# Kernel tuning notes

Hardware: AMD Instinct MI355X
Metric: run time of the kernel (lower is better)

Reference implementation:

```python
import jax, jax.numpy as jnp
import numpy as np

HEAD, STACK = 8, 2
EPS = 1e-5


def _ln2d(x):
    # F.layer_norm(x, x.size()[1:]): normalize over (seq, feature) jointly, no affine
    m = jnp.mean(x, axis=(1, 2), keepdims=True)
    v = jnp.var(x, axis=(1, 2), keepdims=True)
    return (x - m) / jnp.sqrt(v + EPS)


def setup_inputs() -> dict:
    key = jax.random.key(0)
    ks = jax.random.split(key, 8)
    B, S, V, E, D, C = 64, 1024, 8000, 200, 200, 31
    g = lambda k, shape, sc: (jax.random.normal(k, shape, jnp.float32) * sc)
    return dict(
        x=jax.random.randint(ks[0], (B, S), 0, V),
        embed=g(ks[1], (V, E), 0.02),
        pos=g(ks[2], (S, E), 0.02),
        Wp=g(ks[3], (E, D), 0.05), bp=jnp.zeros((D,), jnp.float32),
        Wm=g(ks[4], (D * HEAD, D), 0.05), bm=jnp.zeros((D,), jnp.float32),
        W1=g(ks[5], (D, D), 0.05), b1=jnp.zeros((D,), jnp.float32),
        W2=g(ks[6], (D, D), 0.05), b2=jnp.zeros((D,), jnp.float32),
        Wd=g(ks[7], (D, C), 0.05), bd=jnp.zeros((C,), jnp.float32),
    )


def reference(x, embed, pos, Wp, bp, Wm, bm, W1, b1, W2, b2, Wd, bd):
    h = embed[x] + pos                       # [B,S,200]
    scale = jnp.sqrt(jnp.asarray(Wp.shape[1], jnp.float32))
    for _ in range(STACK):                   # weights shared across stacks (aliased in torch)
        r = h
        p = h @ Wp + bp                      # q = k = v (same aliased Linear in torch)
        a = jax.nn.softmax(jnp.einsum('bsd,btd->bst', p, p) / scale, axis=-1)
        c = jnp.einsum('bst,btd->bsd', a, p)  # [B,S,200]
        cat = jnp.tile(c, (1, 1, HEAD))       # all heads identical -> concat = tile
        h = _ln2d(cat @ Wm + bm + r)
        r = h
        ff = jax.nn.relu(h @ W1 + b1) @ W2 + b2
        h = _ln2d(ff + r)
    return h[:, -1, :] @ Wd + bd             # [B, class_num]; dropout = identity (eval)
```

## Files before the change

### kernel.cpp

```cpp
#include <hip/hip_runtime.h>
#include <cstddef>
#include <cstdint>
#include <cmath>

#define BDIM  64
#define SDIM  1024
#define DDIM  200
#define DPAD  224
#define PSTRIDE 232
#define CDIM  31
#define NSTACK 2
#define EPS   1e-5f
#define LN_N  204800.0f

typedef __attribute__((ext_vector_type(8))) short short8;
typedef __attribute__((ext_vector_type(4))) short short4_t;
typedef __attribute__((ext_vector_type(4))) float f32x4;

__device__ __forceinline__ short f2bf(float f) {
    union { float f; unsigned u; } v; v.f = f;
    unsigned r = v.u + 0x7FFFu + ((v.u >> 16) & 1u);
    return (short)(r >> 16);
}
__device__ __forceinline__ float bf2f(short s) {
    union { unsigned u; float f; } v; v.u = ((unsigned)(unsigned short)s) << 16;
    return v.f;
}
__device__ __forceinline__ unsigned cvtpk_bf16(float a, float b) {
    unsigned r;
    asm volatile("v_cvt_pk_bf16_f32 %0, %1, %2" : "=v"(r) : "v"(a), "v"(b));
    return r;
}
__device__ __forceinline__ void gload_lds16(const short* g, short* l) {
    __builtin_amdgcn_global_load_lds(
        (const __attribute__((address_space(1))) void*)g,
        (__attribute__((address_space(3))) void*)l, 16, 0, 0);
}

__global__ void prep_kernel(const float* __restrict__ Wp, const float* __restrict__ bp,
                            const float* __restrict__ Wm, const float* __restrict__ bm,
                            const float* __restrict__ W1, const float* __restrict__ b1,
                            const float* __restrict__ W2, const float* __restrict__ b2,
                            short* __restrict__ WtP, short* __restrict__ WtM,
                            short* __restrict__ Wt1, short* __restrict__ Wt2,
                            float* __restrict__ bpP, float* __restrict__ bmP,
                            float* __restrict__ b1P, float* __restrict__ b2P,
                            float* __restrict__ csP, float* __restrict__ cs1)
{
    int idx = blockIdx.x * 256 + threadIdx.x;
    if (idx >= DPAD * DPAD) return;
    int n = idx / DPAD, k = idx - n * DPAD;
    bool valid = (n < DDIM) && (k < DDIM);
    WtP[idx] = valid ? f2bf(Wp[(size_t)k * DDIM + n]) : 0;
    Wt1[idx] = valid ? f2bf(W1[(size_t)k * DDIM + n]) : 0;
    Wt2[idx] = valid ? f2bf(W2[(size_t)k * DDIM + n]) : 0;
    float s = 0.f;
    if (valid) {
        #pragma unroll
        for (int blk = 0; blk < 8; ++blk)
            s += Wm[(size_t)(blk * DDIM + k) * DDIM + n];
    }
    WtM[idx] = valid ? f2bf(s) : 0;
    if (idx < DPAD) {
        bpP[idx] = idx < DDIM ? bp[idx] : 0.f;
        bmP[idx] = idx < DDIM ? bm[idx] : 0.f;
        b1P[idx] = idx < DDIM ? b1[idx] : 0.f;
        b2P[idx] = idx < DDIM ? b2[idx] : 0.f;
        float sp = 0.f, s1 = 0.f;
        if (idx < DDIM) {
            for (int kk = 0; kk < DDIM; ++kk) {
                sp += bf2f(f2bf(Wp[(size_t)kk * DDIM + idx]));
                s1 += bf2f(f2bf(W1[(size_t)kk * DDIM + idx]));
            }
        }
        csP[idx] = sp;
        cs1[idx] = s1;
    }
}

__global__ void embed_kernel(const int* __restrict__ x, const float* __restrict__ embed,
                             const float* __restrict__ pos, short* __restrict__ h)
{
    const int row = blockIdx.x;
    const int n = threadIdx.x;
    if (n >= DPAD) return;
    const int s = row & (SDIM - 1);
    const int tok = x[row];
    float v = (n < DDIM) ? embed[(size_t)tok * DDIM + n] + pos[(size_t)s * DDIM + n] : 0.f;
    h[(size_t)row * DPAD + n] = (n < DDIM) ? f2bf(v) : (short)0;
}

#define WSLICE 7168
#define GBUFSZ 11264
__global__ __launch_bounds__(256, 2)
void gemm_bf(const short* __restrict__ act, const float* __restrict__ actParts,
             const short* __restrict__ Wt, const float* __restrict__ bias,
             const float* __restrict__ csW,
             const short* __restrict__ res, const float* __restrict__ resParts,
             short* __restrict__ out, float* __restrict__ parts,
             int doRelu, int outStride)
{
    __shared__ short SB[2][GBUFSZ];

    const int tid  = threadIdx.x;
    const int wave = tid >> 6, lane = tid & 63;
    const int lo   = lane & 15, hi = lane >> 4;
    const int mblk = blockIdx.x * 128;

    auto stage = [&](int ks, int buf) {
        for (int c = wave; c < 22; c += 4) {
            if (c < 14) {
                int row = c * 16 + (lane >> 2);
                int kc  = (lane & 3) ^ ((row >> 1) & 3);
                gload_lds16(Wt + (size_t)row * DPAD + ks * 32 + kc * 8,
                            &SB[buf][c * 512 + lane * 8]);
            } else {
                int ci  = c - 14;
                int row = ci * 16 + (lane >> 2);
                int kc  = (lane & 3) ^ ((row >> 1) & 3);
                gload_lds16(act + (size_t)(mblk + row) * DPAD + ks * 32 + kc * 8,
                            &SB[buf][WSLICE + ci * 512 + lane * 8]);
            }
        }
    };

    f32x4 acc[2][14];
    #pragma unroll
    for (int mt = 0; mt < 2; ++mt)
        #pragma unroll
        for (int nt = 0; nt < 14; ++nt) acc[mt][nt] = (f32x4){0.f, 0.f, 0.f, 0.f};

    stage(0, 0);
    __syncthreads();

    #pragma unroll
    for (int ks = 0; ks < 7; ++ks) {
        const int cur = ks & 1;
        if (ks < 6) stage(ks + 1, cur ^ 1);

        short8 af[2];
        #pragma unroll
        for (int mt = 0; mt < 2; ++mt) {
            int arow = wave * 32 + mt * 16 + lo;
            af[mt] = *(const short8*)&SB[cur][WSLICE + arow * 32
                                             + ((hi * 8) ^ (((arow >> 1) & 3) << 3))];
        }
        #pragma unroll
        for (int nt = 0; nt < 14; ++nt) {
            int brow = nt * 16 + lo;
            short8 bf_ = *(const short8*)&SB[cur][brow * 32
                                                 + ((hi * 8) ^ (((brow >> 1) & 3) << 3))];
            acc[0][nt] = __builtin_amdgcn_mfma_f32_16x16x32_bf16(af[0], bf_, acc[0][nt], 0, 0, 0);
            acc[1][nt] = __builtin_amdgcn_mfma_f32_16x16x32_bf16(af[1], bf_, acc[1][nt], 0, 0, 0);
        }
        __syncthreads();
    }

    const int bb = mblk >> 10;
    float inv_a = 1.f, corr = 0.f;
    if (actParts) {
        float mean = actParts[bb * 2] / LN_N;
        inv_a = rsqrtf(actParts[bb * 2 + 1] / LN_N - mean * mean + EPS);
        corr = mean * inv_a;
    }
    float mean_r = 0.f, inv_r = 1.f;
    if (resParts) {
        mean_r = resParts[bb * 2] / LN_N;
        inv_r = rsqrtf(resParts[bb * 2 + 1] / LN_N - mean_r * mean_r + EPS);
    }

    float s = 0.f, s2 = 0.f;
    #pragma unroll
    for (int mt = 0; mt < 2; ++mt) {
        #pragma unroll
        for (int nt = 0; nt < 14; ++nt) {
            const int n = nt * 16 + lo;
            const float bn = bias[n];
            const float cw = actParts ? csW[n] : 0.f;
            float v[4];
            #pragma unroll
            for (int r = 0; r < 4; ++r)
                v[r] = acc[mt][nt][r] * inv_a + bn - corr * cw;
            if (res) {
                #pragma unroll
                for (int r = 0; r < 4; ++r) {
                    int m = mblk + wave * 32 + mt * 16 + hi * 4 + r;
                    v[r] += (bf2f(res[(size_t)m * DPAD + n]) - mean_r) * inv_r;
                }
            }
            if (doRelu)
                #pragma unroll
                for (int r = 0; r < 4; ++r) v[r] = fmaxf(v[r], 0.f);
            if (n >= DDIM)
                #pragma unroll
                for (int r = 0; r < 4; ++r) v[r] = 0.f;
            if (parts)
                #pragma unroll
                for (int r = 0; r < 4; ++r) { s += v[r]; s2 = fmaf(v[r], v[r], s2); }
            #pragma unroll
            for (int r = 0; r < 4; ++r) {
                int m = mblk + wave * 32 + mt * 16 + hi * 4 + r;
                out[(size_t)m * outStride + n] = f2bf(v[r]);
            }
        }
    }

    if (parts) {
        __shared__ float rs[4], rq[4];
        #pragma unroll
        for (int off = 32; off; off >>= 1) {
            s  += __shfl_down(s, off);
            s2 += __shfl_down(s2, off);
        }
        if (lane == 0) { rs[wave] = s; rq[wave] = s2; }
        __syncthreads();
        if (tid == 0) {
            atomicAdd(&parts[bb * 2],     rs[0] + rs[1] + rs[2] + rs[3]);
            atomicAdd(&parts[bb * 2 + 1], rq[0] + rq[1] + rq[2] + rq[3]);
        }
    }
}

__global__ void vt_kernel(const short* __restrict__ p, short* __restrict__ pt)
{
    __shared__ short T[32][33];
    const int b  = blockIdx.z;
    const int s0 = blockIdx.x * 32;
    const int d0 = blockIdx.y * 32;
    const int t  = threadIdx.x;
    const int row = t >> 3, c4 = (t & 7) * 4;
    short4_t v = *(const short4_t*)(p + ((size_t)b * SDIM + s0 + row) * PSTRIDE + d0 + c4);
    #pragma unroll
    for (int j = 0; j < 4; ++j) T[row][c4 + j] = v[j];
    __syncthreads();
    short4_t o;
    #pragma unroll
    for (int j = 0; j < 4; ++j) o[j] = T[c4 + j][row];
    *(short4_t*)(pt + ((size_t)b * DPAD + d0 + row) * SDIM + s0 + c4) = o;
}

__global__ __launch_bounds__(256, 2)
void attn_kernel(const short* __restrict__ pbf, const short* __restrict__ pt,
                 short* __restrict__ c, float qscale)
{
    __shared__ short Kbuf[2][7680];
    __shared__ short Vbuf[2][6656];

    const int bid = blockIdx.x;
    const int wg  = (bid & 7) * 64 + (bid >> 3);
    const int b   = wg >> 3;
    const int q0  = (wg & 7) * 128;

    const int tid  = threadIdx.x;
    const int wave = tid >> 6;
    const int lane = tid & 63;
    const int lo   = lane & 15;
    const int hi   = lane >> 4;

    const short* pb  = pbf + (size_t)b * SDIM * PSTRIDE;
    const short* ptb = pt  + (size_t)b * DPAD * SDIM;

    auto stage = [&](int kt2, int bufIdx) {
        const short* ks = pb + (size_t)kt2 * 32 * PSTRIDE + lane * 8;
        #pragma unroll
        for (int i = 0; i < 15; ++i)
            gload_lds16(ks + i * 512, &Kbuf[bufIdx][i * 512]);
        #pragma unroll
        for (int i = 0; i < 13; ++i) {
            int e = i * 512 + lane * 8;
            int d = e >> 5;
            int cc = (e & 31) ^ (((d >> 1) & 3) << 3);
            gload_lds16(ptb + (size_t)d * SDIM + kt2 * 32 + cc, &Vbuf[bufIdx][i * 512]);
        }
    };

    short8 qf[2][7];
    #pragma unroll
    for (int qt = 0; qt < 2; ++qt)
        #pragma unroll
        for (int ks = 0; ks < 7; ++ks) {
            short8 q = *(const short8*)(pb + (size_t)(q0 + wave * 32 + qt * 16 + lo) * PSTRIDE
                                        + ks * 32 + hi * 8);
            short8 qs;
            #pragma unroll
            for (int j = 0; j < 8; ++j) qs[j] = f2bf(bf2f(q[j]) * qscale);
            qf[qt][ks] = qs;
        }

    f32x4 o[2][13];
    float m[2], ell[2];
    #pragma unroll
    for (int qt = 0; qt < 2; ++qt) {
        #pragma unroll
        for (int n = 0; n < 13; ++n) o[qt][n] = (f32x4){0.f, 0.f, 0.f, 0.f};
        m[qt] = -1e30f; ell[qt] = 0.f;
    }

    if (wave == 0) stage(0, 0);
    __syncthreads();

    for (int kt = 0; kt < 32; ++kt) {
        const int cur = kt & 1;
        if (kt < 31 && wave == ((kt + 1) & 3)) stage(kt + 1, cur ^ 1);

        f32x4 sacc[2][2];
        #pragma unroll
        for (int qt = 0; qt < 2; ++qt)
            #pragma unroll
            for (int t = 0; t < 2; ++t) sacc[qt][t] = (f32x4){0.f, 0.f, 0.f, 0.f};
        __builtin_amdgcn_s_setprio(1);
        #pragma unroll
        for (int t = 0; t < 2; ++t)
            #pragma unroll
            for (int ks = 0; ks < 7; ++ks) {
                short8 kf = *(const short8*)(&Kbuf[cur][(t * 16 + lo) * PSTRIDE + ks * 32 + hi * 8]);
                sacc[0][t] = __builtin_amdgcn_mfma_f32_16x16x32_bf16(kf, qf[0][ks], sacc[0][t], 0, 0, 0);
                sacc[1][t] = __builtin_amdgcn_mfma_f32_16x16x32_bf16(kf, qf[1][ks], sacc[1][t], 0, 0, 0);
            }
        __builtin_amdgcn_s_setprio(0);

        short8 pa[2];
        #pragma unroll
        for (int qt = 0; qt < 2; ++qt) {
            float mx = fmaxf(fmaxf(fmaxf(sacc[qt][0][0], sacc[qt][0][1]),
                                   fmaxf(sacc[qt][0][2], sacc[qt][0][3])),
                             fmaxf(fmaxf(sacc[qt][1][0], sacc[qt][1][1]),
                                   fmaxf(sacc[qt][1][2], sacc[qt][1][3])));
            mx = fmaxf(mx, __shfl_xor(mx, 16));
            mx = fmaxf(mx, __shfl_xor(mx, 32));
            if (__any(mx > m[qt] + 11.5f)) {
                float mn = fmaxf(m[qt], mx);
                float al = exp2f(m[qt] - mn);
                m[qt] = mn; ell[qt] *= al;
                float alr[4];
                #pragma unroll
                for (int r = 0; r < 4; ++r) alr[r] = __shfl(al, hi * 4 + r);
                #pragma unroll
                for (int n = 0; n < 13; ++n)
                    #pragma unroll
                    for (int r = 0; r < 4; ++r) o[qt][n][r] *= alr[r];
            }
            float p[2][4]; float rsum = 0.f;
            #pragma unroll
            for (int t = 0; t < 2; ++t)
                #pragma unroll
                for (int r = 0; r < 4; ++r) {
                    p[t][r] = exp2f(sacc[qt][t][r] - m[qt]);
                    rsum += p[t][r];
                }
            rsum += __shfl_xor(rsum, 16);
            rsum += __shfl_xor(rsum, 32);
            ell[qt] += rsum;
            unsigned pk01_0 = cvtpk_bf16(p[0][0], p[0][1]);
            unsigned pk23_0 = cvtpk_bf16(p[0][2], p[0][3]);
            unsigned pk01_1 = cvtpk_bf16(p[1][0], p[1][1]);
            unsigned pk23_1 = cvtpk_bf16(p[1][2], p[1][3]);
            const int srcA = lo + ((hi & 1) * 2) * 16;
            const int srcB = srcA + 16;
            int a0 = __shfl((int)pk01_0, srcA), a1 = __shfl((int)pk01_1, srcA);
            int b0 = __shfl((int)pk23_0, srcA), b1 = __shfl((int)pk23_1, srcA);
            int c0 = __shfl((int)pk01_0, srcB), c1 = __shfl((int)pk01_1, srcB);
            int d0 = __shfl((int)pk23_0, srcB), d1 = __shfl((int)pk23_1, srcB);
            const bool thi = (hi >> 1) != 0;
            union { short8 s; int u[4]; } pu;
            pu.u[0] = thi ? a1 : a0;
            pu.u[1] = thi ? b1 : b0;
            pu.u[2] = thi ? c1 : c0;
            pu.u[3] = thi ? d1 : d0;
            pa[qt] = pu.s;
        }

        __builtin_amdgcn_s_setprio(1);
        #pragma unroll
        for (int n = 0; n < 13; ++n) {
            int d = n * 16 + lo;
            int addr = d * 32 + ((hi * 8) ^ (((d >> 1) & 3) << 3));
            short8 vf = *(const short8*)(&Vbuf[cur][addr]);
            o[0][n] = __builtin_amdgcn_mfma_f32_16x16x32_bf16(pa[0], vf, o[0][n], 0, 0, 0);
            o[1][n] = __builtin_amdgcn_mfma_f32_16x16x32_bf16(pa[1], vf, o[1][n], 0, 0, 0);
        }
        __builtin_amdgcn_s_setprio(0);

        __syncthreads();
    }

    #pragma unroll
    for (int qt = 0; qt < 2; ++qt) {
        float inv_l = 1.f / ell[qt];
        float invr[4];
        #pragma unroll
        for (int r = 0; r < 4; ++r) invr[r] = __shfl(inv_l, hi * 4 + r);
        #pragma unroll
        for (int n = 0; n < 13; ++n) {
            int dcol = n * 16 + lo;
            #pragma unroll
            for (int r = 0; r < 4; ++r) {
                size_t row = (size_t)b * SDIM + q0 + wave * 32 + qt * 16 + hi * 4 + r;
                c[row * DPAD + dcol] = f2bf(o[qt][n][r] * invr[r]);
            }
        }
        #pragma unroll
        for (int r = 0; r < 4; ++r) {
            size_t row = (size_t)b * SDIM + q0 + wave * 32 + qt * 16 + hi * 4 + r;
            c[row * DPAD + 208 + lo] = 0;
        }
    }
}

__global__ void final_kernel(const short* __restrict__ y, const float* __restrict__ parts,
                             const float* __restrict__ Wd, const float* __restrict__ bd,
                             float* __restrict__ out)
{
    const int b = blockIdx.x;
    const float sum = parts[b * 2], sq = parts[b * 2 + 1];
    const float mean = sum / LN_N;
    const float inv  = rsqrtf(sq / LN_N - mean * mean + EPS);
    __shared__ float hrow[DDIM];
    const short* row = y + ((size_t)b * SDIM + SDIM - 1) * DPAD;
    for (int d = threadIdx.x; d < DDIM; d += blockDim.x)
        hrow[d] = (bf2f(row[d]) - mean) * inv;
    __syncthreads();
    if (threadIdx.x < CDIM) {
        float acc = bd[threadIdx.x];
        for (int d = 0; d < DDIM; ++d)
            acc = fmaf(hrow[d], Wd[(size_t)d * CDIM + threadIdx.x], acc);
        out[(size_t)b * CDIM + threadIdx.x] = acc;
    }
}

extern "C" void kernel_launch(void* const* d_in, const int* in_sizes, int n_in,
                              void* d_out, int out_size, void* d_ws, size_t ws_size,
                              hipStream_t stream)
{
    const int*   x     = (const int*)  d_in[0];
    const float* embed = (const float*)d_in[1];
    const float* pos   = (const float*)d_in[2];
    const float* Wp    = (const float*)d_in[3];
    const float* bp    = (const float*)d_in[4];
    const float* Wm    = (const float*)d_in[5];
    const float* bm    = (const float*)d_in[6];
    const float* W1    = (const float*)d_in[7];
    const float* b1    = (const float*)d_in[8];
    const float* W2    = (const float*)d_in[9];
    const float* b2    = (const float*)d_in[10];
    const float* Wd    = (const float*)d_in[11];
    const float* bd    = (const float*)d_in[12];
    float* out = (float*)d_out;

    const size_t HB = (size_t)BDIM * SDIM * DPAD;
    const size_t PB = (size_t)BDIM * SDIM * PSTRIDE;

    short* h_bf  = (short*)d_ws;
    short* p_bf  = h_bf  + HB;
    short* pt    = p_bf  + PB;
    short* cb_bf = pt    + HB;
    short* yA    = cb_bf + HB;
    short* yB    = yA    + HB;
    short* WtP   = yB + HB;
    short* WtM   = WtP + DPAD * DPAD;
    short* Wt1   = WtM + DPAD * DPAD;
    short* Wt2   = Wt1 + DPAD * DPAD;
    float* bpP   = (float*)(Wt2 + DPAD * DPAD);
    float* bmP   = bpP + DPAD;
    float* b1P   = bmP + DPAD;
    float* b2P   = b1P + DPAD;
    float* csP   = b2P + DPAD;
    float* cs1   = csP + DPAD;
    float* parts = cs1 + DPAD;
    const size_t need = (size_t)((char*)(parts + 4 * BDIM * 2) - (char*)d_ws);
    if (ws_size < need) return;

    float* pA1 = parts;
    float* pB1 = parts + BDIM * 2;
    float* pA2 = parts + 2 * BDIM * 2;
    float* pB2 = parts + 3 * BDIM * 2;

    prep_kernel<<<dim3((DPAD * DPAD + 255) / 256), dim3(256), 0, stream>>>(
        Wp, bp, Wm, bm, W1, b1, W2, b2, WtP, WtM, Wt1, Wt2, bpP, bmP, b1P, b2P, csP, cs1);
    embed_kernel<<<dim3(BDIM * SDIM), dim3(256), 0, stream>>>(x, embed, pos, h_bf);
    hipMemsetAsync(parts, 0, 4 * BDIM * 2 * sizeof(float), stream);

    const float qscale = 1.44269504f / sqrtf((float)DDIM);
    const dim3 tgrid(SDIM / 32, DPAD / 32, BDIM);

    gemm_bf<<<dim3(512), dim3(256), 0, stream>>>(h_bf, nullptr, WtP, bpP, nullptr,
                                                 nullptr, nullptr, p_bf, nullptr, 0, PSTRIDE);
    vt_kernel<<<tgrid, dim3(256), 0, stream>>>(p_bf, pt);
    attn_kernel<<<dim3(512), dim3(256), 0, stream>>>(p_bf, pt, cb_bf, qscale);
    gemm_bf<<<dim3(512), dim3(256), 0, stream>>>(cb_bf, nullptr, WtM, bmP, nullptr,
                                                 h_bf, nullptr, yA, pA1, 0, DPAD);
    gemm_bf<<<dim3(512), dim3(256), 0, stream>>>(yA, pA1, Wt1, b1P, cs1,
                                                 nullptr, nullptr, cb_bf, nullptr, 1, DPAD);
    gemm_bf<<<dim3(512), dim3(256), 0, stream>>>(cb_bf, nullptr, Wt2, b2P, nullptr,
                                                 yA, pA1, yB, pB1, 0, DPAD);
    gemm_bf<<<dim3(512), dim3(256), 0, stream>>>(yB, pB1, WtP, bpP, csP,
                                                 nullptr, nullptr, p_bf, nullptr, 0, PSTRIDE);
    vt_kernel<<<tgrid, dim3(256), 0, stream>>>(p_bf, pt);
    attn_kernel<<<dim3(512), dim3(256), 0, stream>>>(p_bf, pt, cb_bf, qscale);
    gemm_bf<<<dim3(512), dim3(256), 0, stream>>>(cb_bf, nullptr, WtM, bmP, nullptr,
                                                 yB, pB1, h_bf, pA2, 0, DPAD);
    gemm_bf<<<dim3(512), dim3(256), 0, stream>>>(h_bf, pA2, Wt1, b1P, cs1,
                                                 nullptr, nullptr, cb_bf, nullptr, 1, DPAD);
    gemm_bf<<<dim3(512), dim3(256), 0, stream>>>(cb_bf, nullptr, Wt2, b2P, nullptr,
                                                 h_bf, pA2, yA, pB2, 0, DPAD);
    final_kernel<<<dim3(BDIM), dim3(64), 0, stream>>>(yA, pB2, Wd, bd, out);
}
```

Before: 436.3 us.

## Load GEMM A-fragments directly from global and vectorize embedding kernel

The GEMM kernel stops staging activation tiles through LDS. Each wave now reads its A fragments straight from global memory, and only the weight slices stay double-buffered in shared memory. This shrinks LDS use, so launch bounds are raised to allow three blocks per CU. The embedding kernel becomes a grid-stride loop over 2048 blocks that does float4 loads and short4 stores instead of one block per row with scalar accesses. The direct global A loads are uncoalesced-ish and give up prefetch overlap, which may stall the MFMA loop.

```diff
diff --git a/kernel.cpp b/kernel.cpp
--- a/kernel.cpp
+++ b/kernel.cpp
@@ -81,18 +81,27 @@
 __global__ void embed_kernel(const int* __restrict__ x, const float* __restrict__ embed,
                              const float* __restrict__ pos, short* __restrict__ h)
 {
-    const int row = blockIdx.x;
-    const int n = threadIdx.x;
-    if (n >= DPAD) return;
-    const int s = row & (SDIM - 1);
-    const int tok = x[row];
-    float v = (n < DDIM) ? embed[(size_t)tok * DDIM + n] + pos[(size_t)s * DDIM + n] : 0.f;
-    h[(size_t)row * DPAD + n] = (n < DDIM) ? f2bf(v) : (short)0;
+    const int total = BDIM * SDIM * (DPAD / 4);
+    for (int i = blockIdx.x * 256 + threadIdx.x; i < total; i += gridDim.x * 256) {
+        const int row = i / (DPAD / 4);
+        const int n0  = (i - row * (DPAD / 4)) * 4;
+        short4_t o;
+        if (n0 >= DDIM) {
+            o[0] = o[1] = o[2] = o[3] = 0;
+        } else {
+            const int s = row & (SDIM - 1);
+            const int tok = x[row];
+            const float4 e  = *(const float4*)(embed + (size_t)tok * DDIM + n0);
+            const float4 p4 = *(const float4*)(pos + (size_t)s * DDIM + n0);
+            o[0] = f2bf(e.x + p4.x); o[1] = f2bf(e.y + p4.y);
+            o[2] = f2bf(e.z + p4.z); o[3] = f2bf(e.w + p4.w);
+        }
+        *(short4_t*)(h + (size_t)row * DPAD + n0) = o;
+    }
 }
 
 #define WSLICE 7168
-#define GBUFSZ 11264
-__global__ __launch_bounds__(256, 2)
+__global__ __launch_bounds__(256, 3)
 void gemm_bf(const short* __restrict__ act, const float* __restrict__ actParts,
              const short* __restrict__ Wt, const float* __restrict__ bias,
              const float* __restrict__ csW,
@@ -100,27 +109,20 @@
              short* __restrict__ out, float* __restrict__ parts,
              int doRelu, int outStride)
 {
-    __shared__ short SB[2][GBUFSZ];
+    __shared__ short WB[2][WSLICE];
 
     const int tid  = threadIdx.x;
     const int wave = tid >> 6, lane = tid & 63;
     const int lo   = lane & 15, hi = lane >> 4;
     const int mblk = blockIdx.x * 128;
+    const int m0   = mblk + wave * 32;
 
     auto stage = [&](int ks, int buf) {
-        for (int c = wave; c < 22; c += 4) {
-            if (c < 14) {
-                int row = c * 16 + (lane >> 2);
-                int kc  = (lane & 3) ^ ((row >> 1) & 3);
-                gload_lds16(Wt + (size_t)row * DPAD + ks * 32 + kc * 8,
-                            &SB[buf][c * 512 + lane * 8]);
-            } else {
-                int ci  = c - 14;
-                int row = ci * 16 + (lane >> 2);
-                int kc  = (lane & 3) ^ ((row >> 1) & 3);
-                gload_lds16(act + (size_t)(mblk + row) * DPAD + ks * 32 + kc * 8,
-                            &SB[buf][WSLICE + ci * 512 + lane * 8]);
-            }
+        for (int c = wave; c < 14; c += 4) {
+            int row = c * 16 + (lane >> 2);
+            int kc  = (lane & 3) ^ ((row >> 1) & 3);
+            gload_lds16(Wt + (size_t)row * DPAD + ks * 32 + kc * 8,
+                        &WB[buf][c * 512 + lane * 8]);
         }
     };
 
@@ -140,16 +142,14 @@
 
         short8 af[2];
         #pragma unroll
-        for (int mt = 0; mt < 2; ++mt) {
-            int arow = wave * 32 + mt * 16 + lo;
-            af[mt] = *(const short8*)&SB[cur][WSLICE + arow * 32
-                                             + ((hi * 8) ^ (((arow >> 1) & 3) << 3))];
-        }
+        for (int mt = 0; mt < 2; ++mt)
+            af[mt] = *(const short8*)(act + (size_t)(m0 + mt * 16 + lo) * DPAD
+                                      + ks * 32 + hi * 8);
         #pragma unroll
         for (int nt = 0; nt < 14; ++nt) {
             int brow = nt * 16 + lo;
-            short8 bf_ = *(const short8*)&SB[cur][brow * 32
-                                                 + ((hi * 8) ^ (((brow >> 1) & 3) << 3))];
+            short8 bf_ = *(const short8*)&WB[cur][brow * 32
+                                                  + ((hi * 8) ^ (((brow >> 1) & 3) << 3))];
             acc[0][nt] = __builtin_amdgcn_mfma_f32_16x16x32_bf16(af[0], bf_, acc[0][nt], 0, 0, 0);
             acc[1][nt] = __builtin_amdgcn_mfma_f32_16x16x32_bf16(af[1], bf_, acc[1][nt], 0, 0, 0);
         }
@@ -184,7 +184,7 @@
             if (res) {
                 #pragma unroll
                 for (int r = 0; r < 4; ++r) {
-                    int m = mblk + wave * 32 + mt * 16 + hi * 4 + r;
+                    int m = m0 + mt * 16 + hi * 4 + r;
                     v[r] += (bf2f(res[(size_t)m * DPAD + n]) - mean_r) * inv_r;
                 }
             }
@@ -199,7 +199,7 @@
                 for (int r = 0; r < 4; ++r) { s += v[r]; s2 = fmaf(v[r], v[r], s2); }
             #pragma unroll
             for (int r = 0; r < 4; ++r) {
-                int m = mblk + wave * 32 + mt * 16 + hi * 4 + r;
+                int m = m0 + mt * 16 + hi * 4 + r;
                 out[(size_t)m * outStride + n] = f2bf(v[r]);
             }
         }
@@ -477,7 +477,7 @@
 
     prep_kernel<<<dim3((DPAD * DPAD + 255) / 256), dim3(256), 0, stream>>>(
         Wp, bp, Wm, bm, W1, b1, W2, b2, WtP, WtM, Wt1, Wt2, bpP, bmP, b1P, b2P, csP, cs1);
-    embed_kernel<<<dim3(BDIM * SDIM), dim3(256), 0, stream>>>(x, embed, pos, h_bf);
+    embed_kernel<<<dim3(2048), dim3(256), 0, stream>>>(x, embed, pos, h_bf);
     hipMemsetAsync(parts, 0, 4 * BDIM * 2 * sizeof(float), stream);
 
     const float qscale = 1.44269504f / sqrtf((float)DDIM);
```

Result: no change. 433.3 us (-0.7%).
